# Performance work log

Hardware: AMD Instinct MI355X
Metric: run time of the kernel (lower is better)

Reference implementation:

```python
import jax, jax.numpy as jnp
import numpy as np

NIN, NOUT = 256, 64

def setup_inputs() -> dict:
    key = jax.random.key(0)
    k1, k2, k3, k4 = jax.random.split(key, 4)
    B, T = 4, 4096
    y = jax.random.normal(k1, (B, T, NIN), dtype=jnp.float32)
    # torch Linear(nin, nout).weight has shape [nout, nin]; store as [nin, nout]
    s = 1.0 / np.sqrt(NIN)
    Wq = jax.random.uniform(k2, (NIN, NOUT), jnp.float32, -s, s)
    Wk = jax.random.uniform(k3, (NIN, NOUT), jnp.float32, -s, s)
    Wv = jax.random.uniform(k4, (NIN, NOUT), jnp.float32, -s, s)
    return {"y": y, "Wq": Wq, "Wk": Wk, "Wv": Wv}

def reference(y, Wq, Wk, Wv):
    T = y.shape[1]
    que = y @ Wq  # [B,T,NOUT]
    key = y @ Wk
    val = y @ Wv
    att = jnp.einsum('bqd,bkd->bqk', que, key)  # [B,T,T]
    causal = jnp.tril(jnp.ones((T, T), dtype=bool))  # True = keep
    att = jnp.where(causal, att, -jnp.inf)
    att = jax.nn.softmax(att / jnp.sqrt(jnp.float32(NOUT)), axis=-1)
    return jnp.einsum('bqk,bkd->bqd', att, val)
```

## Files before the change

### kernel.cpp

```cpp
#include <hip/hip_runtime.h>
#include <hip/hip_bf16.h>

#define TLEN 4096
#define NINP 256
#define DD   64

#define QSCALE 0.18033688011112042f

typedef __attribute__((ext_vector_type(8))) short bf16x8;
typedef __attribute__((ext_vector_type(4))) short bf16x4;
typedef __attribute__((ext_vector_type(4))) float f32x4;

union U8 { bf16x8 v; uint u[4]; };
union U4 { bf16x4 v; uint u[2]; };

__device__ inline ushort bfu(float x) {
    union { float f; uint u; } a; a.f = x;
    uint r = a.u + 0x7fffu + ((a.u >> 16) & 1u);
    return (ushort)(r >> 16);
}
__device__ inline uint pk2(float lo, float hi) {
    return (uint)bfu(lo) | ((uint)bfu(hi) << 16);
}
__device__ inline uint cvtpk(float lo, float hi) {
    uint r;
    asm("v_cvt_pk_bf16_f32 %0, %1, %2" : "=v"(r) : "v"(lo), "v"(hi));
    return r;
}

__device__ inline bf16x8 ld16(const ushort* p) {
    return *(const bf16x8*)p;
}

__global__ __launch_bounds__(256) void prep_wt(
    const float* __restrict__ Wq, const float* __restrict__ Wk,
    const float* __restrict__ Wv, ushort* __restrict__ WTf)
{
    __shared__ ushort lt[256 * 66];
    const int t = threadIdx.x;
    const int m = blockIdx.x;
    const float* W = (m == 0) ? Wq : ((m == 1) ? Wk : Wv);
    const float scale = (m == 0) ? QSCALE : 1.0f;

    #pragma unroll
    for (int j = 0; j < 16; ++j) {
        int i4 = t + 256 * j;
        float4 v = *(const float4*)&W[i4 * 4];
        int k = i4 >> 4, d = (i4 * 4) & 63;
        *(uint*)&lt[k * 66 + d]     = pk2(v.x * scale, v.y * scale);
        *(uint*)&lt[k * 66 + d + 2] = pk2(v.z * scale, v.w * scale);
    }
    __syncthreads();
    #pragma unroll
    for (int j = 0; j < 8; ++j) {
        int slot = t + 256 * j;
        int u = slot >> 6, ln = slot & 63;
        int s = u >> 2, nt = u & 3;
        int d = nt * 16 + (ln & 15);
        int k0 = s * 32 + (ln >> 4) * 8;
        uint a0 = (uint)lt[(k0 + 0) * 66 + d] | ((uint)lt[(k0 + 1) * 66 + d] << 16);
        uint a1 = (uint)lt[(k0 + 2) * 66 + d] | ((uint)lt[(k0 + 3) * 66 + d] << 16);
        uint a2 = (uint)lt[(k0 + 4) * 66 + d] | ((uint)lt[(k0 + 5) * 66 + d] << 16);
        uint a3 = (uint)lt[(k0 + 6) * 66 + d] | ((uint)lt[(k0 + 7) * 66 + d] << 16);
        ushort* gd = WTf + m * 16384 + slot * 8;
        ((uint2*)gd)[0] = uint2{a0, a1};
        ((uint2*)gd)[1] = uint2{a2, a3};
    }
}

__global__ __launch_bounds__(256) void qkv_kernel(
    const float* __restrict__ y, const ushort* __restrict__ WTf,
    ushort* __restrict__ Qh, ushort* __restrict__ Kp, ushort* __restrict__ Vp,
    const int rbn)
{
    __shared__ ushort tb[64 * 68];

    const int t = threadIdx.x;
    const int w = t >> 6, lane = t & 63;
    const int quad = lane >> 4, l15 = lane & 15;
    const int mb = blockIdx.x / rbn;
    const int rb = blockIdx.x % rbn;
    const int rowbase = rb * 64;
    const int myrow = rowbase + w * 16 + l15;

    bf16x8 afrag[8];
    const float* yrow = y + (size_t)myrow * NINP;
    #pragma unroll
    for (int s = 0; s < 8; ++s) {
        float4 lo = *(const float4*)&yrow[s * 32 + quad * 8];
        float4 hi = *(const float4*)&yrow[s * 32 + quad * 8 + 4];
        U8 u;
        u.u[0] = pk2(lo.x, lo.y);
        u.u[1] = pk2(lo.z, lo.w);
        u.u[2] = pk2(hi.x, hi.y);
        u.u[3] = pk2(hi.z, hi.w);
        afrag[s] = u.v;
    }

    f32x4 acc[4];
    #pragma unroll
    for (int nt = 0; nt < 4; ++nt) acc[nt] = f32x4{0.f, 0.f, 0.f, 0.f};

    const ushort* Wm = WTf + mb * 16384 + lane * 8;
    #pragma unroll
    for (int s = 0; s < 8; ++s)
        #pragma unroll
        for (int nt = 0; nt < 4; ++nt) {
            bf16x8 bfrag = ld16(Wm + (s * 4 + nt) * 512);
            acc[nt] = __builtin_amdgcn_mfma_f32_16x16x32_bf16(
                afrag[s], bfrag, acc[nt], 0, 0, 0);
        }

    if (mb == 0) {
        #pragma unroll
        for (int nt = 0; nt < 4; ++nt)
            #pragma unroll
            for (int r = 0; r < 4; ++r)
                tb[(w * 16 + quad * 4 + r) * 68 + nt * 16 + l15] = bfu(acc[nt][r]);
        __syncthreads();
        int row = t >> 2, seg = t & 3;
        ushort* gd = Qh + (size_t)(rowbase + row) * DD + seg * 16;
        const ushort* sp = &tb[row * 68 + seg * 16];
        #pragma unroll
        for (int j = 0; j < 4; ++j) ((uint2*)gd)[j] = ((const uint2*)sp)[j];
    } else if (mb == 1) {
        #pragma unroll
        for (int nt = 0; nt < 4; ++nt)
            #pragma unroll
            for (int r = 0; r < 4; ++r)
                tb[(w * 16 + quad * 4 + r) * 68 + nt * 16 + l15] = bfu(acc[nt][r]);
        __syncthreads();
        #pragma unroll
        for (int j = 0; j < 2; ++j) {
            int idx = t + 256 * j;
            int instr = idx >> 6, ln = idx & 63;
            int kt = instr >> 1, s = instr & 1;
            int q2 = ln >> 4, l15b = ln & 15;
            int row = kt * 16 + l15b, dcol = s * 32 + q2 * 8;
            const ushort* sp = &tb[row * 68 + dcol];
            ushort* gd = Kp + (size_t)rb * 4096 + idx * 8;
            ((uint2*)gd)[0] = ((const uint2*)sp)[0];
            ((uint2*)gd)[1] = ((const uint2*)sp)[1];
        }
    } else {
        #pragma unroll
        for (int nt = 0; nt < 4; ++nt) {
            int d = nt * 16 + l15;
            #pragma unroll
            for (int r = 0; r < 4; r += 2) {
                int tt = w * 16 + quad * 4 + r;
                *(uint*)&tb[d * 68 + tt] = pk2(acc[nt][r], acc[nt][r + 1]);
            }
        }
        __syncthreads();
        #pragma unroll
        for (int j = 0; j < 2; ++j) {
            int idx = t + 256 * j;
            int instr = idx >> 6, ln = idx & 63;
            int nt = instr >> 1, m = instr & 1;
            int q2 = ln >> 4, l15b = ln & 15;
            int d = nt * 16 + l15b;
            int k0 = 32 * m + q2 * 4;
            ushort* gd = Vp + (size_t)rb * 4096 + idx * 8;
            ((uint2*)gd)[0] = *(const uint2*)&tb[d * 68 + k0];
            ((uint2*)gd)[1] = *(const uint2*)&tb[d * 68 + k0 + 16];
        }
    }
}

__device__ inline void load_k32(bf16x8 (&kf)[2][2], const ushort* __restrict__ Kw,
                                int ci)
{
    const ushort* base = Kw + (size_t)ci * 2048;
    #pragma unroll
    for (int kt = 0; kt < 2; ++kt)
        #pragma unroll
        for (int s = 0; s < 2; ++s)
            kf[kt][s] = ld16(base + (kt * 2 + s) * 512);
}

__device__ inline void load_v32(U4 (&vt)[4][2], const ushort* __restrict__ Vw,
                                int ci)
{
    const ushort* base = Vw + (size_t)(ci >> 1) * 4096 + (ci & 1) * 512;
    #pragma unroll
    for (int nt = 0; nt < 4; ++nt) {
        U8 uu; uu.v = ld16(base + nt * 1024);
        vt[nt][0].u[0] = uu.u[0]; vt[nt][0].u[1] = uu.u[1];
        vt[nt][1].u[0] = uu.u[2]; vt[nt][1].u[1] = uu.u[3];
    }
}

__device__ inline void chunk32(
    const bf16x8 (&kf)[2][2], bf16x8 (&kfn)[2][2],
    const ushort* __restrict__ Kw, const ushort* __restrict__ Vw,
    const bf16x8 (&qf)[2][2], f32x4 (&oT)[2][4], float (&l_acc)[2],
    int ci, int pf, int chi, int qb, int quad, int l15)
{
    const int c0 = ci * 32;
    U4 vt[4][2];
    load_v32(vt, Vw, ci);

    f32x4 st[2][2];
    #pragma unroll
    for (int qt = 0; qt < 2; ++qt)
        #pragma unroll
        for (int kt = 0; kt < 2; ++kt)
            st[qt][kt] = f32x4{0.f, 0.f, 0.f, 0.f};
    __builtin_amdgcn_s_setprio(1);
    #pragma unroll
    for (int s = 0; s < 2; ++s)
        #pragma unroll
        for (int qt = 0; qt < 2; ++qt)
            #pragma unroll
            for (int kt = 0; kt < 2; ++kt)
                st[qt][kt] = __builtin_amdgcn_mfma_f32_16x16x32_bf16(
                    kf[kt][s], qf[qt][s], st[qt][kt], 0, 0, 0);
    __builtin_amdgcn_s_setprio(0);

    if (pf < chi) load_k32(kfn, Kw, pf);

    U4 pa[2][2];
    if (c0 + 31 <= qb) {
        #pragma unroll
        for (int qt = 0; qt < 2; ++qt)
            #pragma unroll
            for (int kt = 0; kt < 2; ++kt) {
                float p0 = exp2f(st[qt][kt][0]);
                float p1 = exp2f(st[qt][kt][1]);
                float p2 = exp2f(st[qt][kt][2]);
                float p3 = exp2f(st[qt][kt][3]);
                l_acc[qt] += (p0 + p1) + (p2 + p3);
                pa[qt][kt].u[0] = cvtpk(p0, p1);
                pa[qt][kt].u[1] = cvtpk(p2, p3);
            }
    } else {
        #pragma unroll
        for (int qt = 0; qt < 2; ++qt) {
            const int q = qb + qt * 16 + l15;
            #pragma unroll
            for (int kt = 0; kt < 2; ++kt) {
                const int kb0 = c0 + kt * 16 + quad * 4;
                float p[4];
                #pragma unroll
                for (int r = 0; r < 4; ++r) {
                    float e = exp2f(st[qt][kt][r]);
                    p[r] = (kb0 + r <= q) ? e : 0.f;
                    l_acc[qt] += p[r];
                }
                pa[qt][kt].u[0] = cvtpk(p[0], p[1]);
                pa[qt][kt].u[1] = cvtpk(p[2], p[3]);
            }
        }
    }

    __builtin_amdgcn_s_setprio(1);
    #pragma unroll
    for (int qt = 0; qt < 2; ++qt)
        #pragma unroll
        for (int nt = 0; nt < 4; ++nt)
            #pragma unroll
            for (int kt = 0; kt < 2; ++kt)
                oT[qt][nt] = __builtin_amdgcn_mfma_f32_16x16x16bf16_1k(
                    vt[nt][kt].v, pa[qt][kt].v, oT[qt][nt], 0, 0, 0);
    __builtin_amdgcn_s_setprio(0);
}

__global__ __launch_bounds__(768, 3) void attn_kernel(
    const ushort* __restrict__ Qh, const ushort* __restrict__ Kp,
    const ushort* __restrict__ Vp, float* __restrict__ out)
{
    __shared__ float Ob[12][32 * 68];
    __shared__ float lb[12][32];

    const int t = threadIdx.x;
    const int w = t >> 6, lane = t & 63;
    const int quad = lane >> 4, l15 = lane & 15;

    const int x  = blockIdx.x & 7;
    const int b  = x >> 1;
    const int pr = (((int)blockIdx.x >> 3) << 1) | (x & 1);

    const ushort* Qb = Qh + (size_t)b * TLEN * DD;
    const ushort* Kw = Kp + (size_t)b * 64 * 4096 + lane * 8;
    const ushort* Vw = Vp + (size_t)b * 64 * 4096 + lane * 8;
    float* outb = out + (size_t)b * TLEN * DD;

    for (int half = 0; half < 2; ++half) {
        const int tile = half ? (127 - pr) : pr;
        const int seg  = half ? (11 - w) : w;
        const int qb   = tile * 32;
        const int nc   = tile + 1;
        const int cps  = (nc + 11) / 12;
        const int clo  = seg * cps;
        const int chi  = (nc < clo + cps) ? nc : (clo + cps);

        f32x4 oT[2][4];
        #pragma unroll
        for (int qt = 0; qt < 2; ++qt)
            #pragma unroll
            for (int nt = 0; nt < 4; ++nt)
                oT[qt][nt] = f32x4{0.f, 0.f, 0.f, 0.f};
        float l_acc[2] = {0.f, 0.f};

        if (clo < chi) {
            bf16x8 qf[2][2];
            #pragma unroll
            for (int qt = 0; qt < 2; ++qt)
                #pragma unroll
                for (int s = 0; s < 2; ++s)
                    qf[qt][s] = ld16(Qb + (size_t)(qb + qt * 16 + l15) * DD + s * 32 + quad * 8);

            bf16x8 kfA[2][2], kfB[2][2];
            load_k32(kfA, Kw, clo);
            if (clo + 1 < chi) load_k32(kfB, Kw, clo + 1);

            for (int ci = clo; ci < chi; ci += 2) {
                chunk32(kfA, kfA, Kw, Vw, qf, oT, l_acc,
                        ci, ci + 2, chi, qb, quad, l15);
                if (ci + 1 < chi)
                    chunk32(kfB, kfB, Kw, Vw, qf, oT, l_acc,
                            ci + 1, ci + 3, chi, qb, quad, l15);
            }

            #pragma unroll
            for (int qt = 0; qt < 2; ++qt) {
                l_acc[qt] += __shfl_xor(l_acc[qt], 16, 64);
                l_acc[qt] += __shfl_xor(l_acc[qt], 32, 64);
            }
        }

        #pragma unroll
        for (int qt = 0; qt < 2; ++qt) {
            #pragma unroll
            for (int nt = 0; nt < 4; ++nt)
                #pragma unroll
                for (int r = 0; r < 4; ++r)
                    Ob[w][(qt * 16 + l15) * 68 + nt * 16 + quad * 4 + r] = oT[qt][nt][r];
            if (quad == 0) lb[w][qt * 16 + l15] = l_acc[qt];
        }
        __syncthreads();

        #pragma unroll
        for (int e = 0; e < 3; ++e) {
            int idx = t + 768 * e;
            if (idx < 2048) {
                int q = idx >> 6, d = idx & 63;
                float s = 0.f, ls = 0.f;
                #pragma unroll
                for (int ww = 0; ww < 12; ++ww) {
                    s += Ob[ww][q * 68 + d];
                    ls += lb[ww][q];
                }
                outb[(size_t)(qb + q) * DD + d] = s * __builtin_amdgcn_rcpf(ls);
            }
        }
        __syncthreads();
    }
}

extern "C" void kernel_launch(void* const* d_in, const int* in_sizes, int n_in,
                              void* d_out, int out_size, void* d_ws, size_t ws_size,
                              hipStream_t stream) {
    const float* y  = (const float*)d_in[0];
    const float* Wq = (const float*)d_in[1];
    const float* Wk = (const float*)d_in[2];
    const float* Wv = (const float*)d_in[3];
    float* outp = (float*)d_out;

    const int rows = in_sizes[0] / NINP;
    const int nb = rows / TLEN;
    const int rbn = rows / 64;

    ushort* WT = (ushort*)d_ws;
    ushort* Qh = WT + 3 * 16384;
    ushort* Kp = Qh + (size_t)rows * DD;
    ushort* Vp = Kp + (size_t)rows * DD;

    prep_wt<<<3, 256, 0, stream>>>(Wq, Wk, Wv, WT);
    qkv_kernel<<<3 * rbn, 256, 0, stream>>>(y, WT, Qh, Kp, Vp, rbn);
    attn_kernel<<<nb * 64, 768, 0, stream>>>(Qh, Kp, Vp, outp);
}
```

Measured before the change: 101.1 us.

## Use 64-row query tiles split across two blocks with separate normalization kernel

The attention kernel now processes 64-query tiles with 8 waves per block instead of 32-query tiles with 12 waves. Each tile's key range is split across two blocks, which write partial numerators and denominators to workspace. A new norm_kernel then sums the two partials and divides. The larger tile reuses each K/V load across four query sub-tiles, but it raises register pressure and adds an extra kernel launch plus a global round trip for the partials.

```diff
diff --git a/kernel.cpp b/kernel.cpp
--- a/kernel.cpp
+++ b/kernel.cpp
@@ -191,171 +191,182 @@
     }
 }
 
-__device__ inline void chunk32(
-    const bf16x8 (&kf)[2][2], bf16x8 (&kfn)[2][2],
-    const ushort* __restrict__ Kw, const ushort* __restrict__ Vw,
-    const bf16x8 (&qf)[2][2], f32x4 (&oT)[2][4], float (&l_acc)[2],
-    int ci, int pf, int chi, int qb, int quad, int l15)
-{
-    const int c0 = ci * 32;
-    U4 vt[4][2];
-    load_v32(vt, Vw, ci);
-
-    f32x4 st[2][2];
-    #pragma unroll
-    for (int qt = 0; qt < 2; ++qt)
-        #pragma unroll
-        for (int kt = 0; kt < 2; ++kt)
-            st[qt][kt] = f32x4{0.f, 0.f, 0.f, 0.f};
-    __builtin_amdgcn_s_setprio(1);
-    #pragma unroll
-    for (int s = 0; s < 2; ++s)
-        #pragma unroll
-        for (int qt = 0; qt < 2; ++qt)
-            #pragma unroll
-            for (int kt = 0; kt < 2; ++kt)
-                st[qt][kt] = __builtin_amdgcn_mfma_f32_16x16x32_bf16(
-                    kf[kt][s], qf[qt][s], st[qt][kt], 0, 0, 0);
-    __builtin_amdgcn_s_setprio(0);
-
-    if (pf < chi) load_k32(kfn, Kw, pf);
-
-    U4 pa[2][2];
-    if (c0 + 31 <= qb) {
-        #pragma unroll
-        for (int qt = 0; qt < 2; ++qt)
-            #pragma unroll
-            for (int kt = 0; kt < 2; ++kt) {
-                float p0 = exp2f(st[qt][kt][0]);
-                float p1 = exp2f(st[qt][kt][1]);
-                float p2 = exp2f(st[qt][kt][2]);
-                float p3 = exp2f(st[qt][kt][3]);
-                l_acc[qt] += (p0 + p1) + (p2 + p3);
-                pa[qt][kt].u[0] = cvtpk(p0, p1);
-                pa[qt][kt].u[1] = cvtpk(p2, p3);
-            }
-    } else {
-        #pragma unroll
-        for (int qt = 0; qt < 2; ++qt) {
-            const int q = qb + qt * 16 + l15;
-            #pragma unroll
-            for (int kt = 0; kt < 2; ++kt) {
-                const int kb0 = c0 + kt * 16 + quad * 4;
-                float p[4];
-                #pragma unroll
-                for (int r = 0; r < 4; ++r) {
-                    float e = exp2f(st[qt][kt][r]);
-                    p[r] = (kb0 + r <= q) ? e : 0.f;
-                    l_acc[qt] += p[r];
-                }
-                pa[qt][kt].u[0] = cvtpk(p[0], p[1]);
-                pa[qt][kt].u[1] = cvtpk(p[2], p[3]);
-            }
-        }
-    }
-
-    __builtin_amdgcn_s_setprio(1);
-    #pragma unroll
-    for (int qt = 0; qt < 2; ++qt)
-        #pragma unroll
-        for (int nt = 0; nt < 4; ++nt)
-            #pragma unroll
-            for (int kt = 0; kt < 2; ++kt)
-                oT[qt][nt] = __builtin_amdgcn_mfma_f32_16x16x16bf16_1k(
-                    vt[nt][kt].v, pa[qt][kt].v, oT[qt][nt], 0, 0, 0);
-    __builtin_amdgcn_s_setprio(0);
-}
-
-__global__ __launch_bounds__(768, 3) void attn_kernel(
+__global__ __launch_bounds__(512, 2) void attn_kernel(
     const ushort* __restrict__ Qh, const ushort* __restrict__ Kp,
-    const ushort* __restrict__ Vp, float* __restrict__ out)
-{
-    __shared__ float Ob[12][32 * 68];
-    __shared__ float lb[12][32];
+    const ushort* __restrict__ Vp, float* __restrict__ part_n,
+    float* __restrict__ part_l)
+{
+    __shared__ float Ob[8][32 * 68];
+    __shared__ float lb[8][32];
 
     const int t = threadIdx.x;
     const int w = t >> 6, lane = t & 63;
     const int quad = lane >> 4, l15 = lane & 15;
 
-    const int x  = blockIdx.x & 7;
-    const int b  = x >> 1;
-    const int pr = (((int)blockIdx.x >> 3) << 1) | (x & 1);
+    const int x = blockIdx.x & 7;
+    const int b = x >> 1;
+    const int h = x & 1;
+    const int u = (int)blockIdx.x >> 3;
 
     const ushort* Qb = Qh + (size_t)b * TLEN * DD;
     const ushort* Kw = Kp + (size_t)b * 64 * 4096 + lane * 8;
     const ushort* Vw = Vp + (size_t)b * 64 * 4096 + lane * 8;
-    float* outb = out + (size_t)b * TLEN * DD;
 
     for (int half = 0; half < 2; ++half) {
-        const int tile = half ? (127 - pr) : pr;
-        const int seg  = half ? (11 - w) : w;
-        const int qb   = tile * 32;
-        const int nc   = tile + 1;
-        const int cps  = (nc + 11) / 12;
+        const int tile = half ? (63 - u) : u;
+        const int seg  = half ? (15 - (h * 8 + w)) : (h * 8 + w);
+        const int qb   = tile * 64;
+        const int nc   = 2 * tile + 2;
+        const int cps  = (nc + 15) >> 4;
         const int clo  = seg * cps;
         const int chi  = (nc < clo + cps) ? nc : (clo + cps);
 
-        f32x4 oT[2][4];
-        #pragma unroll
-        for (int qt = 0; qt < 2; ++qt)
+        f32x4 oT[4][4];
+        #pragma unroll
+        for (int qt = 0; qt < 4; ++qt)
             #pragma unroll
             for (int nt = 0; nt < 4; ++nt)
                 oT[qt][nt] = f32x4{0.f, 0.f, 0.f, 0.f};
-        float l_acc[2] = {0.f, 0.f};
+        float l_acc[4] = {0.f, 0.f, 0.f, 0.f};
 
         if (clo < chi) {
-            bf16x8 qf[2][2];
-            #pragma unroll
-            for (int qt = 0; qt < 2; ++qt)
+            bf16x8 qf[4][2];
+            #pragma unroll
+            for (int qt = 0; qt < 4; ++qt)
                 #pragma unroll
                 for (int s = 0; s < 2; ++s)
                     qf[qt][s] = ld16(Qb + (size_t)(qb + qt * 16 + l15) * DD + s * 32 + quad * 8);
 
-            bf16x8 kfA[2][2], kfB[2][2];
-            load_k32(kfA, Kw, clo);
-            if (clo + 1 < chi) load_k32(kfB, Kw, clo + 1);
-
-            for (int ci = clo; ci < chi; ci += 2) {
-                chunk32(kfA, kfA, Kw, Vw, qf, oT, l_acc,
-                        ci, ci + 2, chi, qb, quad, l15);
-                if (ci + 1 < chi)
-                    chunk32(kfB, kfB, Kw, Vw, qf, oT, l_acc,
-                            ci + 1, ci + 3, chi, qb, quad, l15);
-            }
-
-            #pragma unroll
-            for (int qt = 0; qt < 2; ++qt) {
+            bf16x8 kf[2][2];
+            load_k32(kf, Kw, clo);
+
+            for (int ci = clo; ci < chi; ++ci) {
+                const int c0 = ci * 32;
+
+                U4 vt[4][2];
+                load_v32(vt, Vw, ci);
+
+                f32x4 st[4][2];
+                #pragma unroll
+                for (int qt = 0; qt < 4; ++qt)
+                    #pragma unroll
+                    for (int kt = 0; kt < 2; ++kt)
+                        st[qt][kt] = f32x4{0.f, 0.f, 0.f, 0.f};
+                __builtin_amdgcn_s_setprio(1);
+                #pragma unroll
+                for (int s = 0; s < 2; ++s)
+                    #pragma unroll
+                    for (int qt = 0; qt < 4; ++qt)
+                        #pragma unroll
+                        for (int kt = 0; kt < 2; ++kt)
+                            st[qt][kt] = __builtin_amdgcn_mfma_f32_16x16x32_bf16(
+                                kf[kt][s], qf[qt][s], st[qt][kt], 0, 0, 0);
+                __builtin_amdgcn_s_setprio(0);
+
+                if (ci + 1 < chi) load_k32(kf, Kw, ci + 1);
+
+                U4 pa[4][2];
+                if (c0 + 31 <= qb) {
+                    #pragma unroll
+                    for (int qt = 0; qt < 4; ++qt)
+                        #pragma unroll
+                        for (int kt = 0; kt < 2; ++kt) {
+                            float p0 = exp2f(st[qt][kt][0]);
+                            float p1 = exp2f(st[qt][kt][1]);
+                            float p2 = exp2f(st[qt][kt][2]);
+                            float p3 = exp2f(st[qt][kt][3]);
+                            l_acc[qt] += (p0 + p1) + (p2 + p3);
+                            pa[qt][kt].u[0] = cvtpk(p0, p1);
+                            pa[qt][kt].u[1] = cvtpk(p2, p3);
+                        }
+                } else {
+                    #pragma unroll
+                    for (int qt = 0; qt < 4; ++qt) {
+                        const int q = qb + qt * 16 + l15;
+                        #pragma unroll
+                        for (int kt = 0; kt < 2; ++kt) {
+                            const int kb0 = c0 + kt * 16 + quad * 4;
+                            float p[4];
+                            #pragma unroll
+                            for (int r = 0; r < 4; ++r) {
+                                float e = exp2f(st[qt][kt][r]);
+                                p[r] = (kb0 + r <= q) ? e : 0.f;
+                                l_acc[qt] += p[r];
+                            }
+                            pa[qt][kt].u[0] = cvtpk(p[0], p[1]);
+                            pa[qt][kt].u[1] = cvtpk(p[2], p[3]);
+                        }
+                    }
+                }
+
+                __builtin_amdgcn_s_setprio(1);
+                #pragma unroll
+                for (int qt = 0; qt < 4; ++qt)
+                    #pragma unroll
+                    for (int nt = 0; nt < 4; ++nt)
+                        #pragma unroll
+                        for (int kt = 0; kt < 2; ++kt)
+                            oT[qt][nt] = __builtin_amdgcn_mfma_f32_16x16x16bf16_1k(
+                                vt[nt][kt].v, pa[qt][kt].v, oT[qt][nt], 0, 0, 0);
+                __builtin_amdgcn_s_setprio(0);
+            }
+
+            #pragma unroll
+            for (int qt = 0; qt < 4; ++qt) {
                 l_acc[qt] += __shfl_xor(l_acc[qt], 16, 64);
                 l_acc[qt] += __shfl_xor(l_acc[qt], 32, 64);
             }
         }
 
-        #pragma unroll
-        for (int qt = 0; qt < 2; ++qt) {
-            #pragma unroll
-            for (int nt = 0; nt < 4; ++nt)
-                #pragma unroll
-                for (int r = 0; r < 4; ++r)
-                    Ob[w][(qt * 16 + l15) * 68 + nt * 16 + quad * 4 + r] = oT[qt][nt][r];
-            if (quad == 0) lb[w][qt * 16 + l15] = l_acc[qt];
-        }
-        __syncthreads();
-
-        #pragma unroll
-        for (int e = 0; e < 3; ++e) {
-            int idx = t + 768 * e;
-            if (idx < 2048) {
+        float* pn = part_n + ((size_t)((b * 64 + tile) * 2 + h)) * 4096;
+        float* pl = part_l + ((size_t)((b * 64 + tile) * 2 + h)) * 64;
+        #pragma unroll
+        for (int pass = 0; pass < 2; ++pass) {
+            #pragma unroll
+            for (int ql = 0; ql < 2; ++ql) {
+                int qt = pass * 2 + ql;
+                #pragma unroll
+                for (int nt = 0; nt < 4; ++nt)
+                    #pragma unroll
+                    for (int r = 0; r < 4; ++r)
+                        Ob[w][(ql * 16 + l15) * 68 + nt * 16 + quad * 4 + r] = oT[qt][nt][r];
+                if (quad == 0) lb[w][ql * 16 + l15] = l_acc[qt];
+            }
+            __syncthreads();
+            #pragma unroll
+            for (int e = 0; e < 4; ++e) {
+                int idx = t + 512 * e;
                 int q = idx >> 6, d = idx & 63;
                 float s = 0.f, ls = 0.f;
                 #pragma unroll
-                for (int ww = 0; ww < 12; ++ww) {
+                for (int ww = 0; ww < 8; ++ww) {
                     s += Ob[ww][q * 68 + d];
                     ls += lb[ww][q];
                 }
-                outb[(size_t)(qb + q) * DD + d] = s * __builtin_amdgcn_rcpf(ls);
-            }
-        }
-        __syncthreads();
+                pn[(pass * 32 + q) * 64 + d] = s;
+                if (d == 0) pl[pass * 32 + q] = ls;
+            }
+            __syncthreads();
+        }
+    }
+}
+
+__global__ __launch_bounds__(256) void norm_kernel(
+    const float* __restrict__ part_n, const float* __restrict__ part_l,
+    float* __restrict__ out)
+{
+    const int bt = blockIdx.x;
+    const size_t n0 = (size_t)bt * 2 * 4096;
+    const size_t l0 = (size_t)bt * 2 * 64;
+    float* ob = out + (size_t)bt * 4096;
+
+    #pragma unroll
+    for (int j = 0; j < 16; ++j) {
+        int idx = threadIdx.x + 256 * j;
+        int q = idx >> 6;
+        float n = part_n[n0 + idx] + part_n[n0 + 4096 + idx];
+        float l = part_l[l0 + q] + part_l[l0 + 64 + q];
+        ob[idx] = n * __builtin_amdgcn_rcpf(l);
     }
 }
 
@@ -369,15 +380,17 @@
     float* outp = (float*)d_out;
 
     const int rows = in_sizes[0] / NINP;
-    const int nb = rows / TLEN;
     const int rbn = rows / 64;
 
     ushort* WT = (ushort*)d_ws;
     ushort* Qh = WT + 3 * 16384;
     ushort* Kp = Qh + (size_t)rows * DD;
     ushort* Vp = Kp + (size_t)rows * DD;
+    float* part_n = (float*)(Vp + (size_t)rows * DD);
+    float* part_l = part_n + (size_t)256 * 2 * 4096;
 
     prep_wt<<<3, 256, 0, stream>>>(Wq, Wk, Wv, WT);
     qkv_kernel<<<3 * rbn, 256, 0, stream>>>(y, WT, Qh, Kp, Vp, rbn);
-    attn_kernel<<<nb * 64, 768, 0, stream>>>(Qh, Kp, Vp, outp);
-}
+    attn_kernel<<<rbn, 512, 0, stream>>>(Qh, Kp, Vp, part_n, part_l);
+    norm_kernel<<<rbn, 256, 0, stream>>>(part_n, part_l, outp);
+}
```

Result: slower. 107.4 us (+6.2%).
